# Kernel tuning notes

Measured on AMD Instinct MI355X. Metric: run time of the kernel, lower is better.

Reference implementation:

```python
import jax, jax.numpy as jnp
import numpy as np

N_NODES = 100000
N_EDGES = 1600000
K_IND = 16          # num_indicator_weight (distance bins)
K_MLP = 16          # num_mlp_weight
DIM_HIDDEN = 64     # dim_mlp_hidden
DIST_MAX = 1.0      # distance_max
K = K_IND + K_MLP   # node feature dim / Dense output dim


def setup_inputs() -> dict:
    key = jax.random.key(0)
    ks = jax.random.split(key, 10)
    nodes = jax.random.normal(ks[0], (N_NODES, K), dtype=jnp.float32)
    distance = jax.random.uniform(ks[1], (N_EDGES,), dtype=jnp.float32) * DIST_MAX
    receivers = jnp.sort(jax.random.randint(ks[2], (N_EDGES,), 0, N_NODES, dtype=jnp.int32))
    senders = jax.random.randint(ks[3], (N_EDGES,), 0, N_NODES, dtype=jnp.int32)
    edges_padding = jnp.ones((N_EDGES,), dtype=jnp.float32)
    # MLPWeights params (Dense(1->H), Dense(H->K_MLP))
    w1 = jax.random.normal(ks[4], (1, DIM_HIDDEN), dtype=jnp.float32) / np.sqrt(1.0)
    b1 = jnp.zeros((DIM_HIDDEN,), dtype=jnp.float32)
    w2 = jax.random.normal(ks[5], (DIM_HIDDEN, K_MLP), dtype=jnp.float32) / np.sqrt(DIM_HIDDEN)
    b2 = jnp.zeros((K_MLP,), dtype=jnp.float32)
    # PowerDifference params (a=0.5, b=2)
    a = jnp.array([0.5], dtype=jnp.float32)
    b = jnp.array([2.0], dtype=jnp.float32)
    # gamma_self (no bias), gamma_gathered (with bias), both Dense(K->K)
    wg_self = jax.random.normal(ks[6], (K, K), dtype=jnp.float32) / np.sqrt(K)
    wg_gath = jax.random.normal(ks[7], (K, K), dtype=jnp.float32) / np.sqrt(K)
    bg_gath = jnp.zeros((K,), dtype=jnp.float32)
    return {"nodes": nodes, "distance": distance, "edges_padding": edges_padding,
            "receivers": receivers, "senders": senders,
            "w1": w1, "b1": b1, "w2": w2, "b2": b2,
            "a": a, "b": b, "wg_self": wg_self, "wg_gath": wg_gath, "bg_gath": bg_gath}


def _normalize_edges(edges, seg_ids, num_segments):
    sums = jax.ops.segment_sum(edges, seg_ids, num_segments=num_segments, indices_are_sorted=True)
    return edges / (sums[seg_ids] + 1e-5)


def _softmax_edges(edges, seg_ids, num_segments):
    maxs = jax.ops.segment_max(edges, seg_ids, num_segments=num_segments, indices_are_sorted=True)
    e = jnp.exp(edges - maxs[seg_ids])
    sums = jax.ops.segment_sum(e, seg_ids, num_segments=num_segments, indices_are_sorted=True)
    return e / sums[seg_ids]


def reference(nodes, distance, edges_padding, receivers, senders,
              w1, b1, w2, b2, a, b, wg_self, wg_gath, bg_gath):
    n = nodes.shape[0]
    d = distance[:, None]                                   # [E,1]
    # IndicatorWeights: bin membership via heaviside of product
    bins = jnp.linspace(0.0, DIST_MAX, K_IND + 1, dtype=nodes.dtype)
    indicator = jnp.heaviside((bins[None, :-1] - d) * (d - bins[None, 1:]), 0.0)  # [E,K_IND]
    indicator_w = _normalize_edges(indicator, receivers, n)
    # MLPWeights: Dense -> relu -> Dense, then segment softmax
    mlp = jax.nn.relu(d @ w1 + b1) @ w2 + b2                # [E,K_MLP]
    mlp_w = _softmax_edges(mlp, receivers, n)
    weights = jnp.concatenate([indicator_w, mlp_w], axis=1) * edges_padding[:, None]  # [E,K]
    # PowerDifference on gathered node pairs
    a_c = jnp.clip(a, 0.0, 1.0)
    b_c = jnp.abs(b)
    edge_pds = jnp.power(jnp.abs(a_c * nodes[receivers] - (1.0 - a_c) * nodes[senders]), b_c)  # [E,K]
    gathered = jax.ops.segment_sum(weights * edge_pds, receivers, num_segments=n, indices_are_sorted=True)  # [N,K]
    out = jax.nn.relu(nodes @ wg_self + (gathered @ wg_gath + bg_gath))
    return out
```

## Files before the change

kernel.cpp:

```cpp
#include <hip/hip_runtime.h>
#include <math.h>

#define K_TOT 32
#define K_IND 16
#define K_MLP 16
#define DHID  64
#define M_NODES 4
#define LOG2E 1.44269504088896340736f

__device__ __forceinline__ float fast_rcp(float x) {
    float r; asm("v_rcp_f32 %0, %1" : "=v"(r) : "v"(x)); return r;
}
__device__ __forceinline__ float fast_exp2(float x) {
    float r; asm("v_exp_f32 %0, %1" : "=v"(r) : "v"(x)); return r;
}


__global__ void prep_kernel(const int* __restrict__ recv, int E, int N,
                            const float* __restrict__ w1,
                            const float* __restrict__ b1,
                            const float* __restrict__ w2,
                            float* __restrict__ wsP,
                            float* __restrict__ wsN,
                            int* __restrict__ wsflag,
                            int* __restrict__ rp) {
    if (blockIdx.x == 0 && threadIdx.x < 64) {
        int t = threadIdx.x;
        if (t < K_MLP) {
            float P = 0.f, Nn = 0.f;
            for (int j = 0; j < DHID; ++j) {
                float w = w1[j];
                float v = w2[j * K_MLP + t];
                P  += fmaxf(w, 0.f) * v;
                Nn += fminf(w, 0.f) * v;
            }
            wsP[t] = P; wsN[t] = Nn;
        }
        bool nz = (b1[t] != 0.f);
        unsigned long long mask = __ballot(nz);
        if (t == 0) *wsflag = (mask == 0ull) ? 1 : 0;
    }
    int tid = blockIdx.x * blockDim.x + threadIdx.x;
    if (tid <= N) {
        int lo = 0, hi = E;
        while (lo < hi) {
            int mid = (lo + hi) >> 1;
            if (recv[mid] < tid) lo = mid + 1; else hi = mid;
        }
        rp[tid] = lo;
    }
}

__global__ __launch_bounds__(256) void graph_kernel(
        const float* __restrict__ nodes,
        const float* __restrict__ dist,
        const float* __restrict__ padv,
        const int*   __restrict__ send,
        const float* __restrict__ w1,
        const float* __restrict__ b1,
        const float* __restrict__ w2,
        const float* __restrict__ b2,
        const float* __restrict__ a_p,
        const float* __restrict__ b_p,
        const float* __restrict__ wg_self,
        const float* __restrict__ wg_gath,
        const float* __restrict__ bg,
        const float* __restrict__ wsP,
        const float* __restrict__ wsN,
        const int*   __restrict__ wsflag,
        const int*   __restrict__ rp,
        float* __restrict__ out,
        int N) {
    __shared__ __align__(16) float2 s_wp[1024];
    __shared__ float2 s_gn[4][32];

    {
        int t = threadIdx.x;
        float4 ws4 = ((const float4*)wg_self)[t];
        float4 wg4 = ((const float4*)wg_gath)[t];
        s_wp[t * 4 + 0] = make_float2(ws4.x, wg4.x);
        s_wp[t * 4 + 1] = make_float2(ws4.y, wg4.y);
        s_wp[t * 4 + 2] = make_float2(ws4.z, wg4.z);
        s_wp[t * 4 + 3] = make_float2(ws4.w, wg4.w);
    }
    __syncthreads();

    int wv   = threadIdx.x >> 6;
    int wave = blockIdx.x * 4 + wv;
    int n0   = wave * M_NODES;
    if (n0 >= N) return;
    int nEndN = n0 + M_NODES; if (nEndN > N) nEndN = N;

    int lane = threadIdx.x & 63;
    int eg   = lane >> 4;
    int cc   = lane & 15;

    float a_c = fminf(fmaxf(a_p[0], 0.f), 1.f);
    float am  = 1.f - a_c;
    float bc  = fabsf(b_p[0]);

    float Pk = wsP[cc];
    float Nk = wsN[cc];
    float Pk2 = Pk * LOG2E;
    float Nk2 = Nk * LOG2E;
    float negM2 = -fmaxf(fabsf(Pk), fabsf(Nk)) * LOG2E;

    float lo = (float)cc * 0.0625f;
    float hi = lo + 0.0625f;

    int fastflag = (*wsflag != 0) && (bc == 2.0f);
    float bgv = bg[lane & 31];

    int h  = lane >> 5;
    int oc = lane & 31;
    const float2* gnp = &s_gn[wv][h * 16];
    const float2* wpp = &s_wp[h * 16 * 32 + oc];

    int e0 = rp[n0];
    for (int n = n0; n < nEndN; ++n) {
        int eEnd = rp[n + 1];
        int len  = eEnd - e0;

        const float* nrow = nodes + n * K_TOT;
        float nr0 = nrow[cc];
        float nr1 = nrow[cc + 16];
        float anr0 = a_c * nr0;
        float anr1 = a_c * nr1;

        float cnt = 0.f, si = 0.f;
        float l = 0.f, acc = 0.f;
        float g_ind, g_mlp;

        if (__builtin_amdgcn_readfirstlane((int)(fastflag && (len <= 64)))) {
            if (len > 0) {
                int idx = (lane < len) ? lane : (len - 1);
                int ei  = e0 + idx;
                float d_all  = dist[ei];
                int   s_all  = send[ei];
                float pe_all = padv[ei];
                d_all = (lane < len) ? d_all : 2.0f;

                int nG = (len + 3) >> 2;

#define GRP_BODY(G)                                                          \
                {                                                            \
                    int i = ((G) << 2) + eg;                                 \
                    bool valid = i < len;                                    \
                    float d  = __shfl(d_all, i);                             \
                    int   s  = __shfl(s_all, i);                             \
                    float pe = __shfl(pe_all, i);                            \
                    const float* nsrow = nodes + (s * K_TOT + cc);           \
                    float ns0 = nsrow[0];                                    \
                    float ns1 = nsrow[16];                                   \
                    float t0 = fmaf(-am, ns0, anr0);                         \
                    float t1 = fmaf(-am, ns1, anr1);                         \
                    float pd0 = t0 * t0;                                     \
                    float pd1 = t1 * t1;                                     \
                    bool inb = (d > lo) && (d < hi);                         \
                    cnt += inb ? 1.f : 0.f;                                  \
                    si   = inb ? fmaf(pe, pd0, si) : si;                     \
                    float q2 = (d > 0.f) ? Pk2 : Nk2;                        \
                    float p = fast_exp2(fmaf(d, q2, negM2));                 \
                    p = valid ? p : 0.f;                                     \
                    l += p;                                                  \
                    acc = fmaf(p, pe * pd1, acc);                            \
                }

                int g = 0;
                for (; g + 2 <= nG; g += 2) {
                    GRP_BODY(g)
                    GRP_BODY(g + 1)
                }
                if (g < nG) {
                    GRP_BODY(g)
                }
#undef GRP_BODY
            }

#pragma unroll
            for (int off = 16; off <= 32; off <<= 1) {
                cnt += __shfl_xor(cnt, off);
                si  += __shfl_xor(si,  off);
                l   += __shfl_xor(l,   off);
                acc += __shfl_xor(acc, off);
            }
            g_ind = si * fast_rcp(cnt + 1e-5f);
            g_mlp = (l > 0.f) ? (acc * fast_rcp(l)) : 0.f;
        } else {
            float m_on = -INFINITY;
            for (int i = eg; i < len; i += 4) {
                int e = e0 + i;
                float d  = dist[e];
                int   s  = send[e];
                float pe = padv[e];
                const float* nsrow = nodes + (s * K_TOT + cc);
                float ns0 = nsrow[0];
                float ns1 = nsrow[16];
                float t0 = fabsf(fmaf(-am, ns0, anr0));
                float t1 = fabsf(fmaf(-am, ns1, anr1));
                float pd0 = powf(t0, bc);
                float pd1 = powf(t1, bc);

                bool inb = (d > lo) && (d < hi);
                cnt += inb ? 1.f : 0.f;
                si  += inb ? pe * pd0 : 0.f;

                float mlp = 0.f;
                for (int j = 0; j < DHID; ++j) {
                    float h2 = fmaxf(fmaf(d, w1[j], b1[j]), 0.f);
                    mlp = fmaf(h2, w2[j * K_MLP + cc], mlp);
                }
                float mn = fmaxf(m_on, mlp);
                float al = (m_on == -INFINITY) ? 0.f : __expf(m_on - mn);
                float p  = __expf(mlp - mn);
                l   = fmaf(l, al, p);
                acc = fmaf(acc, al, p * pe * pd1);
                m_on = mn;
            }
#pragma unroll
            for (int off = 16; off <= 32; off <<= 1) {
                cnt += __shfl_xor(cnt, off);
                si  += __shfl_xor(si,  off);
                float m2 = __shfl_xor(m_on, off), l2 = __shfl_xor(l, off), a2 = __shfl_xor(acc, off);
                float mn = fmaxf(m_on, m2);
                float f1 = (m_on == -INFINITY) ? 0.f : __expf(m_on - mn);
                float f2 = (m2   == -INFINITY) ? 0.f : __expf(m2 - mn);
                l   = l * f1 + l2 * f2;
                acc = acc * f1 + a2 * f2;
                m_on = mn;
            }
            g_ind = si / (cnt + 1e-5f);
            g_mlp = (l > 0.f) ? (acc / l) : 0.f;
        }

        float pre_g = ((lane >> 4) & 1) ? g_mlp : g_ind;
        float pre_n = ((lane >> 4) & 1) ? nr1 : nr0;
        if (lane < 32) s_gn[wv][lane] = make_float2(pre_n, pre_g);

        float o = 0.f;
#pragma unroll
        for (int jj = 0; jj < 16; ++jj) {
            float2 v = gnp[jj];
            float2 w = wpp[jj * 32];
            o = fmaf(v.x, w.x, o);
            o = fmaf(v.y, w.y, o);
        }
        o += __shfl_xor(o, 32);
        if (h == 0) {
            out[n * K_TOT + oc] = fmaxf(o + bgv, 0.f);
        }

        e0 = eEnd;
    }
}

extern "C" void kernel_launch(void* const* d_in, const int* in_sizes, int n_in,
                              void* d_out, int out_size, void* d_ws, size_t ws_size,
                              hipStream_t stream) {
    const float* nodes   = (const float*)d_in[0];
    const float* dist    = (const float*)d_in[1];
    const float* padv    = (const float*)d_in[2];
    const int*   recv    = (const int*)d_in[3];
    const int*   send    = (const int*)d_in[4];
    const float* w1      = (const float*)d_in[5];
    const float* b1      = (const float*)d_in[6];
    const float* w2      = (const float*)d_in[7];
    const float* b2      = (const float*)d_in[8];
    const float* a_p     = (const float*)d_in[9];
    const float* b_p     = (const float*)d_in[10];
    const float* wg_self = (const float*)d_in[11];
    const float* wg_gath = (const float*)d_in[12];
    const float* bg      = (const float*)d_in[13];
    float* out = (float*)d_out;

    int N = in_sizes[0] / K_TOT;
    int E = in_sizes[1];

    float* wsf    = (float*)d_ws;
    float* wsP    = wsf;
    float* wsN    = wsf + 16;
    int*   wsflag = (int*)d_ws + 32;
    int*   rp     = (int*)d_ws + 64;

    prep_kernel<<<(N + 1 + 255) / 256, 256, 0, stream>>>(recv, E, N, w1, b1, w2,
                                                         wsP, wsN, wsflag, rp);
    int waves = (N + M_NODES - 1) / M_NODES;
    graph_kernel<<<(waves + 3) / 4, 256, 0, stream>>>(
        nodes, dist, padv, send, w1, b1, w2, b2, a_p, b_p,
        wg_self, wg_gath, bg, wsP, wsN, wsflag, rp, out, N);
}
```

Baseline: 156.6 us.

## Batch per-wave node processing with prefetched edges and fused 4-node output matmul

Row pointers are now built by scanning edge boundaries once per edge instead of a binary search per node. In the main kernel, each wave loads all five row offsets and the node rows for its four nodes up front. The fast path prefetches the next node's edge data while the current node is being reduced. The output Dense layer is batched over the four nodes, so shared-memory weight reads are shared and stores are coalesced, which removes the serial per-node dependency chain. The price is more registers and a larger shared buffer, and the change relies on every node needing at most 64 edges for the fast path.

Result: faster. 147.7 us (-5.7%).

```diff
diff --git a/kernel.cpp b/kernel.cpp
--- a/kernel.cpp
+++ b/kernel.cpp
@@ -40,14 +40,14 @@
         unsigned long long mask = __ballot(nz);
         if (t == 0) *wsflag = (mask == 0ull) ? 1 : 0;
     }
-    int tid = blockIdx.x * blockDim.x + threadIdx.x;
-    if (tid <= N) {
-        int lo = 0, hi = E;
-        while (lo < hi) {
-            int mid = (lo + hi) >> 1;
-            if (recv[mid] < tid) lo = mid + 1; else hi = mid;
-        }
-        rp[tid] = lo;
+    int e = blockIdx.x * blockDim.x + threadIdx.x;
+    if (e < E) {
+        int r0 = recv[e];
+        int r1 = (e + 1 < E) ? recv[e + 1] : N;
+        if (e == 0) {
+            for (int t = 0; t <= r0; ++t) rp[t] = 0;
+        }
+        for (int t = r0 + 1; t <= r1; ++t) rp[t] = e + 1;
     }
 }
 
@@ -70,9 +70,9 @@
         const int*   __restrict__ wsflag,
         const int*   __restrict__ rp,
         float* __restrict__ out,
-        int N) {
+        int N, int E) {
     __shared__ __align__(16) float2 s_wp[1024];
-    __shared__ float2 s_gn[4][32];
+    __shared__ __align__(16) float2 s_gn[4][32][4];
 
     {
         int t = threadIdx.x;
@@ -89,7 +89,6 @@
     int wave = blockIdx.x * 4 + wv;
     int n0   = wave * M_NODES;
     if (n0 >= N) return;
-    int nEndN = n0 + M_NODES; if (nEndN > N) nEndN = N;
 
     int lane = threadIdx.x & 63;
     int eg   = lane >> 4;
@@ -103,7 +102,7 @@
     float Nk = wsN[cc];
     float Pk2 = Pk * LOG2E;
     float Nk2 = Nk * LOG2E;
-    float negM2 = -fmaxf(fabsf(Pk), fabsf(Nk)) * LOG2E;
+    float negM2 = -fmaxf(fabsf(Pk2), fabsf(Nk2));
 
     float lo = (float)cc * 0.0625f;
     float hi = lo + 0.0625f;
@@ -111,35 +110,52 @@
     int fastflag = (*wsflag != 0) && (bc == 2.0f);
     float bgv = bg[lane & 31];
 
-    int h  = lane >> 5;
-    int oc = lane & 31;
-    const float2* gnp = &s_gn[wv][h * 16];
-    const float2* wpp = &s_wp[h * 16 * 32 + oc];
-
-    int e0 = rp[n0];
-    for (int n = n0; n < nEndN; ++n) {
-        int eEnd = rp[n + 1];
-        int len  = eEnd - e0;
-
-        const float* nrow = nodes + n * K_TOT;
-        float nr0 = nrow[cc];
-        float nr1 = nrow[cc + 16];
-        float anr0 = a_c * nr0;
-        float anr1 = a_c * nr1;
-
-        float cnt = 0.f, si = 0.f;
-        float l = 0.f, acc = 0.f;
-        float g_ind, g_mlp;
-
-        if (__builtin_amdgcn_readfirstlane((int)(fastflag && (len <= 64)))) {
+    int rl = rp[min(n0 + min(lane, 4), N)];
+    int e0k[5];
+#pragma unroll
+    for (int k = 0; k < 5; ++k) e0k[k] = __shfl(rl, k);
+    int lenk[4]; int maxlen = 0;
+#pragma unroll
+    for (int k = 0; k < 4; ++k) {
+        lenk[k] = e0k[k + 1] - e0k[k];
+        maxlen = max(maxlen, lenk[k]);
+    }
+
+    int cap = N * K_TOT - 1;
+    float rowA = nodes[min(n0 * K_TOT + lane, cap)];
+    float rowB = nodes[min(n0 * K_TOT + 64 + lane, cap)];
+
+    float nr0k[4], nr1k[4];
+
+    if (__builtin_amdgcn_readfirstlane((int)(fastflag && (maxlen <= 64)))) {
+        float dC, peC; int sC;
+        {
+            int li = min(lane, max(lenk[0] - 1, 0));
+            int ei = min(e0k[0] + li, E - 1);
+            dC = dist[ei]; sC = send[ei]; peC = padv[ei];
+        }
+#pragma unroll
+        for (int k = 0; k < 4; ++k) {
+            float dNx = 0.f, peNx = 0.f; int sNx = 0;
+            if (k < 3) {
+                int li = min(lane, max(lenk[k + 1] - 1, 0));
+                int ei = min(e0k[k + 1] + li, E - 1);
+                dNx = dist[ei]; sNx = send[ei]; peNx = padv[ei];
+            }
+            int len = lenk[k];
+            float d_all  = (lane < len) ? dC : 2.0f;
+            int   s_all  = sC;
+            float pe_all = peC;
+
+            float nsrc = (k < 2) ? rowA : rowB;
+            float nr0 = __shfl(nsrc, (k & 1) * 32 + cc);
+            float nr1 = __shfl(nsrc, (k & 1) * 32 + cc + 16);
+            nr0k[k] = nr0; nr1k[k] = nr1;
+            float anr0 = a_c * nr0;
+            float anr1 = a_c * nr1;
+
+            float cnt = 0.f, si = 0.f, l = 0.f, acc = 0.f;
             if (len > 0) {
-                int idx = (lane < len) ? lane : (len - 1);
-                int ei  = e0 + idx;
-                float d_all  = dist[ei];
-                int   s_all  = send[ei];
-                float pe_all = padv[ei];
-                d_all = (lane < len) ? d_all : 2.0f;
-
                 int nG = (len + 3) >> 2;
 
 #define GRP_BODY(G)                                                          \
@@ -184,9 +200,25 @@
                 l   += __shfl_xor(l,   off);
                 acc += __shfl_xor(acc, off);
             }
-            g_ind = si * fast_rcp(cnt + 1e-5f);
-            g_mlp = (l > 0.f) ? (acc * fast_rcp(l)) : 0.f;
-        } else {
+            float g_ind = si * fast_rcp(cnt + 1e-5f);
+            float g_mlp = (l > 0.f) ? (acc * fast_rcp(l)) : 0.f;
+
+            float pre_g = ((lane >> 4) & 1) ? g_mlp : g_ind;
+            float pre_n = ((lane >> 4) & 1) ? nr1 : nr0;
+            if (lane < 32) s_gn[wv][lane][k] = make_float2(pre_n, pre_g);
+
+            dC = dNx; sC = sNx; peC = peNx;
+        }
+    } else {
+        for (int k = 0; k < 4; ++k) {
+            int len = lenk[k], e0 = e0k[k];
+            float nsrc = (k < 2) ? rowA : rowB;
+            float nr0 = __shfl(nsrc, (k & 1) * 32 + cc);
+            float nr1 = __shfl(nsrc, (k & 1) * 32 + cc + 16);
+            float anr0 = a_c * nr0;
+            float anr1 = a_c * nr1;
+
+            float cnt = 0.f, si = 0.f, l = 0.f, acc = 0.f;
             float m_on = -INFINITY;
             for (int i = eg; i < len; i += 4) {
                 int e = e0 + i;
@@ -229,29 +261,47 @@
                 acc = acc * f1 + a2 * f2;
                 m_on = mn;
             }
-            g_ind = si / (cnt + 1e-5f);
-            g_mlp = (l > 0.f) ? (acc / l) : 0.f;
-        }
-
-        float pre_g = ((lane >> 4) & 1) ? g_mlp : g_ind;
-        float pre_n = ((lane >> 4) & 1) ? nr1 : nr0;
-        if (lane < 32) s_gn[wv][lane] = make_float2(pre_n, pre_g);
-
-        float o = 0.f;
-#pragma unroll
-        for (int jj = 0; jj < 16; ++jj) {
-            float2 v = gnp[jj];
-            float2 w = wpp[jj * 32];
-            o = fmaf(v.x, w.x, o);
-            o = fmaf(v.y, w.y, o);
-        }
-        o += __shfl_xor(o, 32);
-        if (h == 0) {
-            out[n * K_TOT + oc] = fmaxf(o + bgv, 0.f);
-        }
-
-        e0 = eEnd;
-    }
+            float g_ind = si / (cnt + 1e-5f);
+            float g_mlp = (l > 0.f) ? (acc / l) : 0.f;
+
+            float pre_g = ((lane >> 4) & 1) ? g_mlp : g_ind;
+            float pre_n = ((lane >> 4) & 1) ? nr1 : nr0;
+            if (lane < 32) s_gn[wv][lane][k] = make_float2(pre_n, pre_g);
+        }
+    }
+
+    int h  = lane >> 5;
+    int oc = lane & 31;
+    const float2* wpp = &s_wp[(h * 16) * K_TOT + oc];
+    const float2* gnp = &s_gn[wv][h * 16][0];
+
+    float o0 = 0.f, o1 = 0.f, o2 = 0.f, o3 = 0.f;
+#pragma unroll
+    for (int jj = 0; jj < 16; ++jj) {
+        float2 w  = wpp[jj * K_TOT];
+        float2 v0 = gnp[jj * 4 + 0];
+        float2 v1 = gnp[jj * 4 + 1];
+        float2 v2 = gnp[jj * 4 + 2];
+        float2 v3 = gnp[jj * 4 + 3];
+        o0 = fmaf(v0.x, w.x, o0); o0 = fmaf(v0.y, w.y, o0);
+        o1 = fmaf(v1.x, w.x, o1); o1 = fmaf(v1.y, w.y, o1);
+        o2 = fmaf(v2.x, w.x, o2); o2 = fmaf(v2.y, w.y, o2);
+        o3 = fmaf(v3.x, w.x, o3); o3 = fmaf(v3.y, w.y, o3);
+    }
+    o0 += __shfl_xor(o0, 32);
+    o1 += __shfl_xor(o1, 32);
+    o2 += __shfl_xor(o2, 32);
+    o3 += __shfl_xor(o3, 32);
+    o0 = fmaxf(o0 + bgv, 0.f);
+    o1 = fmaxf(o1 + bgv, 0.f);
+    o2 = fmaxf(o2 + bgv, 0.f);
+    o3 = fmaxf(o3 + bgv, 0.f);
+
+    float st0 = (lane >= 32) ? o1 : o0;
+    float st1 = (lane >= 32) ? o3 : o2;
+    int   b5  = lane >> 5;
+    if (n0 + b5 < N)     out[n0 * K_TOT + lane]      = st0;
+    if (n0 + 2 + b5 < N) out[n0 * K_TOT + 64 + lane] = st1;
 }
 
 extern "C" void kernel_launch(void* const* d_in, const int* in_sizes, int n_in,
@@ -282,10 +332,10 @@
     int*   wsflag = (int*)d_ws + 32;
     int*   rp     = (int*)d_ws + 64;
 
-    prep_kernel<<<(N + 1 + 255) / 256, 256, 0, stream>>>(recv, E, N, w1, b1, w2,
-                                                         wsP, wsN, wsflag, rp);
+    prep_kernel<<<(E + 255) / 256, 256, 0, stream>>>(recv, E, N, w1, b1, w2,
+                                                     wsP, wsN, wsflag, rp);
     int waves = (N + M_NODES - 1) / M_NODES;
     graph_kernel<<<(waves + 3) / 4, 256, 0, stream>>>(
         nodes, dist, padv, send, w1, b1, w2, b2, a_p, b_p,
-        wg_self, wg_gath, bg, wsP, wsN, wsflag, rp, out, N);
-}
+        wg_self, wg_gath, bg, wsP, wsN, wsflag, rp, out, N, E);
+}
```
